# Optimization experiments

Measured on AMD Instinct MI355X. Metric: run time of the kernel, lower is better.

## Reference

```python
import jax, jax.numpy as jnp
import numpy as np

N = 100000      # nodes
E = 1600000     # edges (avg degree 16)
EMB = 64        # embedding_size (per-head out channels)
H = 2           # heads (hardcoded in module)
HID = 128       # hidden_size
NEG_SLOPE = 0.2 # GATv2 default


def setup_inputs() -> dict:
    key = jax.random.key(0)
    ks = jax.random.split(key, 12)
    s = 0.1
    x = jax.random.normal(ks[0], (N, 1), jnp.float32)
    edge_index = jax.random.randint(ks[1], (2, E), 0, N, dtype=jnp.int64)
    edge_attr = jax.random.normal(ks[2], (E, 1), jnp.float32)
    # GATv2Conv params (in_channels=1, out=EMB, heads=H, edge_dim=1)
    W_l = jax.random.normal(ks[3], (1, H * EMB), jnp.float32) * s
    b_l = jnp.zeros((H * EMB,), jnp.float32)
    W_r = jax.random.normal(ks[4], (1, H * EMB), jnp.float32) * s
    b_r = jnp.zeros((H * EMB,), jnp.float32)
    W_e = jax.random.normal(ks[5], (1, H * EMB), jnp.float32) * s   # lin_edge, bias=False
    att = jax.random.normal(ks[6], (H, EMB), jnp.float32) * s       # attention vector a
    bias_out = jnp.zeros((H * EMB,), jnp.float32)                   # conv output bias (concat=True)
    # fc: Linear(embedding_size*4, hidden_size)
    W_fc = jax.random.normal(ks[7], (HID, 4 * EMB), jnp.float32) * s
    b_fc = jnp.zeros((HID,), jnp.float32)
    return {
        "x": x, "edge_index": edge_index, "edge_attr": edge_attr,
        "target_node_idx": 123,
        "W_l": W_l, "b_l": b_l, "W_r": W_r, "b_r": b_r,
        "W_e": W_e, "att": att, "bias_out": bias_out,
        "W_fc": W_fc, "b_fc": b_fc,
    }


def reference(x, edge_index, edge_attr, target_node_idx,
              W_l, b_l, W_r, b_r, W_e, att, bias_out, W_fc, b_fc):
    n = x.shape[0]
    h, c = att.shape
    src, dst = edge_index[0], edge_index[1]

    # add_self_loops with fill_value='mean': per-target-node mean of incoming edge_attr
    deg = jax.ops.segment_sum(jnp.ones((src.shape[0],), x.dtype), dst, num_segments=n)
    attr_mean = jax.ops.segment_sum(edge_attr, dst, num_segments=n) / jnp.maximum(deg, 1.0)[:, None]
    loop = jnp.arange(n, dtype=src.dtype)
    src_f = jnp.concatenate([src, loop])
    dst_f = jnp.concatenate([dst, loop])
    ea = jnp.concatenate([edge_attr, attr_mean], axis=0)  # [E+N, 1]

    # per-head node transforms
    x_l = (x @ W_l + b_l).reshape(n, h, c)  # source transform
    x_r = (x @ W_r + b_r).reshape(n, h, c)  # target transform
    e_edge = (ea @ W_e).reshape(-1, h, c)   # edge-feature transform

    # GATv2: e_ij = a^T LeakyReLU(W_l x_j + W_r x_i + W_e e_ij)
    e = jax.nn.leaky_relu(x_l[src_f] + x_r[dst_f] + e_edge, NEG_SLOPE)  # [E', H, C]
    logits = jnp.einsum('ehc,hc->eh', e, att)  # [E', H]

    # segment softmax over incoming edges per target node
    m = jax.ops.segment_max(logits, dst_f, num_segments=n)     # [N, H]
    expv = jnp.exp(logits - m[dst_f])
    denom = jax.ops.segment_sum(expv, dst_f, num_segments=n)
    alpha = expv / denom[dst_f]                                 # [E', H]

    # weighted scatter-aggregate of source messages, concat heads, add bias
    out = jax.ops.segment_sum(alpha[:, :, None] * x_l[src_f], dst_f, num_segments=n)
    graph_emb = out.reshape(n, h * c) + bias_out                # [N, 2*EMB]

    # gather target, repeat, concat, linear
    tgt = graph_emb[target_node_idx]                            # [2*EMB]
    combined = jnp.concatenate([graph_emb, jnp.broadcast_to(tgt[None, :], graph_emb.shape)], axis=1)
    return combined @ W_fc.T + b_fc                             # [N, HID]
```

## Files before the change

### kernel.cpp

```cpp
#include <hip/hip_runtime.h>
#include <math.h>


#define LRELU_A1 0.6f
#define LRELU_A2 0.4f
#define NPB       512
#define NPB_SHIFT 9
#define EPB      2048
#define TB_BIN    512
#define CAP_MAX    24

__global__ void k_prep(const unsigned int* __restrict__ ei,
                       const float* __restrict__ att,
                       const float* __restrict__ W_l,
                       const float* __restrict__ b_l, const float* __restrict__ b_r,
                       const float* __restrict__ bias_out,
                       const float* __restrict__ W_fc, const float* __restrict__ b_fc,
                       float* __restrict__ C) {
  int j = threadIdx.x;
  unsigned long long nz = __ballot(j < 32 && ei[2 * j + 1] != 0u);
  if (j == 0) ((int*)C)[1024] = (nz == 0ull) ? 1 : 0;
  if (j >= 128) return;
  float a = att[j];
  C[j] = LRELU_A1 * a;
  C[128 + j] = LRELU_A2 * a;
  C[256 + j] = b_l[j] + b_r[j];
  const float* wrow = W_fc + j * 256;
  float u0 = 0.f, u1 = 0.f, v0 = 0.f, v1 = 0.f, cb = b_fc[j];
  for (int c = 0; c < 64; c++) {
    u0 = fmaf(W_l[c],      wrow[c],       u0);
    u1 = fmaf(W_l[64 + c], wrow[64 + c],  u1);
    v0 = fmaf(W_l[c],      wrow[128 + c], v0);
    v1 = fmaf(W_l[64 + c], wrow[192 + c], v1);
  }
  for (int t = 0; t < 128; t++) {
    float gb = b_l[t] + bias_out[t];
    cb = fmaf(gb, wrow[t] + wrow[128 + t], cb);
  }
  C[384 + j] = u0;
  C[512 + j] = u1;
  C[640 + j] = v0;
  C[768 + j] = v1;
  C[896 + j] = cb;
}

#define CH_STEP(comp, ACC, i)                                                      \
  do {                                                                             \
    float v_ = fmaf(xs4[i], wl.comp, fmaf(xt4[i], wr.comp, fmaf(ae4[i], we.comp, bb.comp))); \
    ACC[i] = fmaf(a2.comp, fabsf(v_), fmaf(a1.comp, v_, ACC[i]));                  \
  } while (0)

__global__ __launch_bounds__(TB_BIN) void k_bin(
    const float* __restrict__ x, const int* __restrict__ ei,
    const float* __restrict__ ea,
    const float* __restrict__ WL, const float* __restrict__ WR,
    const float* __restrict__ WE, const float* __restrict__ C,
    int4* __restrict__ rec, unsigned char* __restrict__ cntm,
    float* __restrict__ acc, int cap, int NB, int SB, int E) {
  __shared__ int cnt[256];
  const int tid = threadIdx.x;
  if (tid < 256) cnt[tid] = 0;
  __syncthreads();

  const int e0 = blockIdx.x * EPB;
  const bool w64 = ((const int*)C)[1024] != 0;
  const float* A1 = C;
  const float* A2 = C + 128;
  const float* BASE = C + 256;

  int de4[4];
  float ae4[4], xs4[4], xt4[4];
  bool ok[4];
#pragma unroll
  for (int i = 0; i < 4; i++) {
    int e = e0 + i * TB_BIN + tid;
    ok[i] = (e < E);
    int ee = ok[i] ? e : 0;
    int s_ = w64 ? ei[2 * ee] : ei[ee];
    int d_ = w64 ? ei[2 * (E + ee)] : ei[E + ee];
    de4[i] = d_;
    ae4[i] = ea[ee];
    xs4[i] = x[s_];
    xt4[i] = x[d_];
  }
  float acc0[4] = {0.f, 0.f, 0.f, 0.f};
  float acc1[4] = {0.f, 0.f, 0.f, 0.f};
#pragma unroll 4
  for (int jb = 0; jb < 64; jb += 4) {
    float4 wl = *(const float4*)(WL + jb);
    float4 wr = *(const float4*)(WR + jb);
    float4 we = *(const float4*)(WE + jb);
    float4 bb = *(const float4*)(BASE + jb);
    float4 a1 = *(const float4*)(A1 + jb);
    float4 a2 = *(const float4*)(A2 + jb);
#pragma unroll
    for (int i = 0; i < 4; i++) {
      CH_STEP(x, acc0, i); CH_STEP(y, acc0, i); CH_STEP(z, acc0, i); CH_STEP(w, acc0, i);
    }
  }
#pragma unroll 4
  for (int jb = 64; jb < 128; jb += 4) {
    float4 wl = *(const float4*)(WL + jb);
    float4 wr = *(const float4*)(WR + jb);
    float4 we = *(const float4*)(WE + jb);
    float4 bb = *(const float4*)(BASE + jb);
    float4 a1 = *(const float4*)(A1 + jb);
    float4 a2 = *(const float4*)(A2 + jb);
#pragma unroll
    for (int i = 0; i < 4; i++) {
      CH_STEP(x, acc1, i); CH_STEP(y, acc1, i); CH_STEP(z, acc1, i); CH_STEP(w, acc1, i);
    }
  }
#pragma unroll
  for (int i = 0; i < 4; i++) {
    if (!ok[i]) continue;
    int d_ = de4[i];
    int b = d_ >> NPB_SHIFT;
    float eh0 = __expf(acc0[i]);
    float eh1 = __expf(acc1[i]);
    int slot = atomicAdd(&cnt[b], 1);
    if (slot < cap) {
      unsigned eab = (__float_as_uint(ae4[i]) & ~511u) | (unsigned)(d_ & 511);
      rec[((size_t)b * SB + blockIdx.x) * cap + slot] =
          make_int4(__float_as_int(eh0), __float_as_int(eh1),
                    __float_as_int(xs4[i]), (int)eab);
    } else {
      float* a = acc + (size_t)d_ * 8;
      atomicAdd(a + 0, eh0);
      atomicAdd(a + 1, eh0 * xs4[i]);
      atomicAdd(a + 2, eh1);
      atomicAdd(a + 3, eh1 * xs4[i]);
      atomicAdd(a + 4, ae4[i]);
      atomicAdd(a + 5, 1.0f);
    }
  }
  __syncthreads();
  if (tid < 64) {
    unsigned w = 0;
#pragma unroll
    for (int k = 0; k < 4; k++) {
      int b = tid * 4 + k;
      unsigned c = (unsigned)min(cnt[b], cap);
      w |= (c & 0xFFu) << (8 * k);
    }
    ((unsigned*)(cntm + (size_t)blockIdx.x * 256))[tid] = w;
  }
}

__global__ __launch_bounds__(256, 4) void k_reduce(
    const int4* __restrict__ rec, const unsigned char* __restrict__ cntm,
    float* __restrict__ part, int cap, int SB) {
  __shared__ float lacc[NPB * 7];
  const int tid = threadIdx.x;
  const int b = blockIdx.x >> 1;
  const int j = blockIdx.x & 1;
  for (int i = tid; i < NPB * 7; i += 256) lacc[i] = 0.f;
  __syncthreads();
  const int sh = (SB + 1) >> 1;
  const int s_end = min(SB, (j + 1) * sh);
  for (int s = j * sh + tid; s < s_end; s += 256) {
    int c = cntm[(size_t)s * 256 + b];
    const int4* cell = rec + ((size_t)b * SB + s) * cap;
    for (int i = 0; i < c; i++) {
      int4 r = cell[i];
      float e0v = __int_as_float(r.x);
      float e1v = __int_as_float(r.y);
      float xsv = __int_as_float(r.z);
      unsigned eab = (unsigned)r.w;
      float* a = lacc + (int)(eab & 511u) * 7;
      float aev = __uint_as_float(eab & ~511u);
      atomicAdd(a + 0, e0v);
      atomicAdd(a + 1, e0v * xsv);
      atomicAdd(a + 2, e1v);
      atomicAdd(a + 3, e1v * xsv);
      atomicAdd(a + 4, aev);
      atomicAdd(a + 5, 1.0f);
    }
  }
  __syncthreads();
  float* dst = part + (size_t)blockIdx.x * (NPB * 6);
  for (int i = tid; i < NPB * 6; i += 256)
    dst[i] = lacc[(i / 6) * 7 + (i % 6)];
}

__global__ __launch_bounds__(256) void k_final(
    const float* __restrict__ x,
    const float* __restrict__ WL, const float* __restrict__ WR,
    const float* __restrict__ WE, const float* __restrict__ C,
    const float* __restrict__ part, const float* __restrict__ acc,
    float* __restrict__ S, int N) {
  int n = blockIdx.x * blockDim.x + threadIdx.x;
  if (n >= N) return;
  int b = n >> NPB_SHIFT;
  int l = n & (NPB - 1);
  const float* p0 = part + ((size_t)(2 * b)     * (NPB * 6)) + l * 6;
  const float* p1 = part + ((size_t)(2 * b + 1) * (NPB * 6)) + l * 6;
  const float* g  = acc + (size_t)n * 8;
  float den0 = p0[0] + p1[0] + g[0];
  float num0 = p0[1] + p1[1] + g[1];
  float den1 = p0[2] + p1[2] + g[2];
  float num1 = p0[3] + p1[3] + g[3];
  float asum = p0[4] + p1[4] + g[4];
  float cntv = p0[5] + p1[5] + g[5];
  const float* A1 = C;
  const float* A2 = C + 128;
  const float* BASE = C + 256;
  float xn = x[n];
  float am = asum / fmaxf(cntv, 1.0f);
  float acc0 = 0.f, acc1 = 0.f;
#pragma unroll 4
  for (int jb = 0; jb < 64; jb += 4) {
    float4 wl = *(const float4*)(WL + jb);
    float4 wr = *(const float4*)(WR + jb);
    float4 we = *(const float4*)(WE + jb);
    float4 bb = *(const float4*)(BASE + jb);
    float4 a1 = *(const float4*)(A1 + jb);
    float4 a2 = *(const float4*)(A2 + jb);
    float v;
    v = fmaf(xn, wl.x + wr.x, fmaf(am, we.x, bb.x)); acc0 = fmaf(a2.x, fabsf(v), fmaf(a1.x, v, acc0));
    v = fmaf(xn, wl.y + wr.y, fmaf(am, we.y, bb.y)); acc0 = fmaf(a2.y, fabsf(v), fmaf(a1.y, v, acc0));
    v = fmaf(xn, wl.z + wr.z, fmaf(am, we.z, bb.z)); acc0 = fmaf(a2.z, fabsf(v), fmaf(a1.z, v, acc0));
    v = fmaf(xn, wl.w + wr.w, fmaf(am, we.w, bb.w)); acc0 = fmaf(a2.w, fabsf(v), fmaf(a1.w, v, acc0));
  }
#pragma unroll 4
  for (int jb = 64; jb < 128; jb += 4) {
    float4 wl = *(const float4*)(WL + jb);
    float4 wr = *(const float4*)(WR + jb);
    float4 we = *(const float4*)(WE + jb);
    float4 bb = *(const float4*)(BASE + jb);
    float4 a1 = *(const float4*)(A1 + jb);
    float4 a2 = *(const float4*)(A2 + jb);
    float v;
    v = fmaf(xn, wl.x + wr.x, fmaf(am, we.x, bb.x)); acc1 = fmaf(a2.x, fabsf(v), fmaf(a1.x, v, acc1));
    v = fmaf(xn, wl.y + wr.y, fmaf(am, we.y, bb.y)); acc1 = fmaf(a2.y, fabsf(v), fmaf(a1.y, v, acc1));
    v = fmaf(xn, wl.z + wr.z, fmaf(am, we.z, bb.z)); acc1 = fmaf(a2.z, fabsf(v), fmaf(a1.z, v, acc1));
    v = fmaf(xn, wl.w + wr.w, fmaf(am, we.w, bb.w)); acc1 = fmaf(a2.w, fabsf(v), fmaf(a1.w, v, acc1));
  }
  float s0 = __expf(acc0), s1 = __expf(acc1);
  float2 sv;
  sv.x = (num0 + s0 * xn) / (den0 + s0);
  sv.y = (num1 + s1 * xn) / (den1 + s1);
  *(float2*)(S + 2 * n) = sv;
}

__global__ __launch_bounds__(256) void k_out(
    const float* __restrict__ S, const float* __restrict__ C,
    const int* __restrict__ tgtp, float* __restrict__ out, int N) {
  int g = blockIdx.x * blockDim.x + threadIdx.x;
  if (g >= N * 32) return;
  int n = g >> 5;
  int kq = (g & 31) * 4;
  int T = tgtp[0];
  float s0t = S[2 * T], s1t = S[2 * T + 1];
  float2 s = *(const float2*)(S + 2 * n);
  float4 u0 = *(const float4*)(C + 384 + kq);
  float4 u1 = *(const float4*)(C + 512 + kq);
  float4 v0 = *(const float4*)(C + 640 + kq);
  float4 v1 = *(const float4*)(C + 768 + kq);
  float4 cb = *(const float4*)(C + 896 + kq);
  float4 o;
  o.x = fmaf(s.x, u0.x, fmaf(s.y, u1.x, fmaf(s0t, v0.x, fmaf(s1t, v1.x, cb.x))));
  o.y = fmaf(s.x, u0.y, fmaf(s.y, u1.y, fmaf(s0t, v0.y, fmaf(s1t, v1.y, cb.y))));
  o.z = fmaf(s.x, u0.z, fmaf(s.y, u1.z, fmaf(s0t, v0.z, fmaf(s1t, v1.z, cb.z))));
  o.w = fmaf(s.x, u0.w, fmaf(s.y, u1.w, fmaf(s0t, v0.w, fmaf(s1t, v1.w, cb.w))));
  *(float4*)(out + n * 128 + kq) = o;
}

extern "C" void kernel_launch(void* const* d_in, const int* in_sizes, int n_in,
                              void* d_out, int out_size, void* d_ws, size_t ws_size,
                              hipStream_t stream) {
  const float* x        = (const float*)d_in[0];
  const int*   ei       = (const int*)d_in[1];
  const float* ea       = (const float*)d_in[2];
  const int*   tgt      = (const int*)d_in[3];
  const float* W_l      = (const float*)d_in[4];
  const float* b_l      = (const float*)d_in[5];
  const float* W_r      = (const float*)d_in[6];
  const float* b_r      = (const float*)d_in[7];
  const float* W_e      = (const float*)d_in[8];
  const float* att      = (const float*)d_in[9];
  const float* bias_out = (const float*)d_in[10];
  const float* W_fc     = (const float*)d_in[11];
  const float* b_fc     = (const float*)d_in[12];

  const int N = in_sizes[0];
  const int E = in_sizes[2];
  const int NB = (N + NPB - 1) / NPB;
  const int SB = (E + EPB - 1) / EPB;

  size_t cnt_bytes  = (size_t)SB * 256;
  size_t part_bytes = (size_t)NB * 2 * NPB * 6 * 4;
  size_t acc_bytes  = (size_t)N * 8 * 4;
  size_t S_bytes    = (size_t)N * 2 * 4;
  size_t C_bytes    = 1152 * 4;
  size_t fixed = cnt_bytes + part_bytes + acc_bytes + S_bytes + C_bytes + 1024;

  int cap = 1;
  if (ws_size > fixed) {
    size_t c = (ws_size - fixed) / ((size_t)NB * SB * 16);
    cap = (int)(c > CAP_MAX ? CAP_MAX : (c < 1 ? 1 : c));
  }

  char* p = (char*)d_ws;
  int4*          rec  = (int4*)p;          p += (size_t)NB * SB * cap * 16;
  unsigned char* cntm = (unsigned char*)p; p += cnt_bytes;
  float*         part = (float*)p;         p += part_bytes;
  float*         acc  = (float*)p;         p += acc_bytes;
  float*         S    = (float*)p;         p += S_bytes;
  float*         C    = (float*)p;

  hipMemsetAsync(acc, 0, acc_bytes, stream);
  k_prep<<<1, 128, 0, stream>>>((const unsigned int*)ei, att, W_l, b_l, b_r,
                                bias_out, W_fc, b_fc, C);
  k_bin<<<SB, TB_BIN, 0, stream>>>(x, ei, ea, W_l, W_r, W_e, C,
                                   rec, cntm, acc, cap, NB, SB, E);
  k_reduce<<<NB * 2, 256, 0, stream>>>(rec, cntm, part, cap, SB);
  k_final<<<(N + 255) / 256, 256, 0, stream>>>(x, W_l, W_r, W_e, C, part, acc, S, N);
  k_out<<<(N * 32 + 255) / 256, 256, 0, stream>>>(S, C, tgt, (float*)d_out, N);
}
```

Before: 240.7 us.

## Stage binned edge records in shared memory and flatten reduce over contiguous slots

k_bin now writes edge records into a shared-memory staging buffer per destination bin, then copies them out to global memory in one coalesced pass per bin, with a transposed count matrix. k_reduce is split four ways per bin and each thread walks a flat range of slots with four loads in flight, instead of one thread per source cell looping over a variable count. k_prep is parallelised across 1024 threads with shuffle reductions. The aim is to replace scattered record writes and divergent, latency-bound reduce loops with coalesced traffic, at the cost of a large shared buffer in k_bin that lowers its occupancy and one extra partial to sum in k_final.

After: 274.0 us. 1.14x slower.

```diff
diff --git a/kernel.cpp b/kernel.cpp
--- a/kernel.cpp
+++ b/kernel.cpp
@@ -8,40 +8,53 @@
 #define NPB_SHIFT 9
 #define EPB      2048
 #define TB_BIN    512
-#define CAP_MAX    24
-
-__global__ void k_prep(const unsigned int* __restrict__ ei,
-                       const float* __restrict__ att,
-                       const float* __restrict__ W_l,
-                       const float* __restrict__ b_l, const float* __restrict__ b_r,
-                       const float* __restrict__ bias_out,
-                       const float* __restrict__ W_fc, const float* __restrict__ b_fc,
-                       float* __restrict__ C) {
-  int j = threadIdx.x;
-  unsigned long long nz = __ballot(j < 32 && ei[2 * j + 1] != 0u);
-  if (j == 0) ((int*)C)[1024] = (nz == 0ull) ? 1 : 0;
-  if (j >= 128) return;
-  float a = att[j];
-  C[j] = LRELU_A1 * a;
-  C[128 + j] = LRELU_A2 * a;
-  C[256 + j] = b_l[j] + b_r[j];
+#define CAPL       24
+#define NBMAX     200
+#define SPLITS      4
+
+__global__ __launch_bounds__(1024) void k_prep(
+    const unsigned int* __restrict__ ei,
+    const float* __restrict__ att, const float* __restrict__ W_l,
+    const float* __restrict__ b_l, const float* __restrict__ b_r,
+    const float* __restrict__ bias_out,
+    const float* __restrict__ W_fc, const float* __restrict__ b_fc,
+    float* __restrict__ C) {
+  int t = threadIdx.x;
+  unsigned long long nz = __ballot(t < 32 && ei[2 * t + 1] != 0u);
+  if (t == 0) ((int*)C)[1024] = (nz == 0ull) ? 1 : 0;
+  int j = t >> 3, q = t & 7;
   const float* wrow = W_fc + j * 256;
-  float u0 = 0.f, u1 = 0.f, v0 = 0.f, v1 = 0.f, cb = b_fc[j];
-  for (int c = 0; c < 64; c++) {
-    u0 = fmaf(W_l[c],      wrow[c],       u0);
-    u1 = fmaf(W_l[64 + c], wrow[64 + c],  u1);
-    v0 = fmaf(W_l[c],      wrow[128 + c], v0);
-    v1 = fmaf(W_l[64 + c], wrow[192 + c], v1);
-  }
-  for (int t = 0; t < 128; t++) {
-    float gb = b_l[t] + bias_out[t];
-    cb = fmaf(gb, wrow[t] + wrow[128 + t], cb);
-  }
-  C[384 + j] = u0;
-  C[512 + j] = u1;
-  C[640 + j] = v0;
-  C[768 + j] = v1;
-  C[896 + j] = cb;
+  float u0 = 0.f, u1 = 0.f, v0 = 0.f, v1 = 0.f, cb = 0.f;
+  for (int c = q; c < 64; c += 8) {
+    float wl0 = W_l[c], wl1 = W_l[64 + c];
+    u0 = fmaf(wl0, wrow[c],       u0);
+    u1 = fmaf(wl1, wrow[64 + c],  u1);
+    v0 = fmaf(wl0, wrow[128 + c], v0);
+    v1 = fmaf(wl1, wrow[192 + c], v1);
+  }
+  for (int c = q; c < 128; c += 8) {
+    float gb = b_l[c] + bias_out[c];
+    cb = fmaf(gb, wrow[c] + wrow[128 + c], cb);
+  }
+#pragma unroll
+  for (int off = 4; off; off >>= 1) {
+    u0 += __shfl_down(u0, off);
+    u1 += __shfl_down(u1, off);
+    v0 += __shfl_down(v0, off);
+    v1 += __shfl_down(v1, off);
+    cb += __shfl_down(cb, off);
+  }
+  if (q == 0) {
+    float a = att[j];
+    C[j]       = LRELU_A1 * a;
+    C[128 + j] = LRELU_A2 * a;
+    C[256 + j] = b_l[j] + b_r[j];
+    C[384 + j] = u0;
+    C[512 + j] = u1;
+    C[640 + j] = v0;
+    C[768 + j] = v1;
+    C[896 + j] = cb + b_fc[j];
+  }
 }
 
 #define CH_STEP(comp, ACC, i)                                                      \
@@ -56,10 +69,11 @@
     const float* __restrict__ WL, const float* __restrict__ WR,
     const float* __restrict__ WE, const float* __restrict__ C,
     int4* __restrict__ rec, unsigned char* __restrict__ cntm,
-    float* __restrict__ acc, int cap, int NB, int SB, int E) {
-  __shared__ int cnt[256];
+    float* __restrict__ acc, int capG, int NB, int SB, int E) {
+  __shared__ int4 stag[NBMAX * CAPL];
+  __shared__ int  cnt[NBMAX];
   const int tid = threadIdx.x;
-  if (tid < 256) cnt[tid] = 0;
+  for (int i = tid; i < NBMAX; i += TB_BIN) cnt[i] = 0;
   __syncthreads();
 
   const int e0 = blockIdx.x * EPB;
@@ -118,12 +132,11 @@
     int b = d_ >> NPB_SHIFT;
     float eh0 = __expf(acc0[i]);
     float eh1 = __expf(acc1[i]);
-    int slot = atomicAdd(&cnt[b], 1);
-    if (slot < cap) {
+    int slot = (b < NBMAX) ? atomicAdd(&cnt[b], 1) : CAPL;
+    if (slot < CAPL) {
       unsigned eab = (__float_as_uint(ae4[i]) & ~511u) | (unsigned)(d_ & 511);
-      rec[((size_t)b * SB + blockIdx.x) * cap + slot] =
-          make_int4(__float_as_int(eh0), __float_as_int(eh1),
-                    __float_as_int(xs4[i]), (int)eab);
+      stag[b * CAPL + slot] = make_int4(__float_as_int(eh0), __float_as_int(eh1),
+                                        __float_as_int(xs4[i]), (int)eab);
     } else {
       float* a = acc + (size_t)d_ * 8;
       atomicAdd(a + 0, eh0);
@@ -135,47 +148,81 @@
     }
   }
   __syncthreads();
-  if (tid < 64) {
-    unsigned w = 0;
-#pragma unroll
-    for (int k = 0; k < 4; k++) {
-      int b = tid * 4 + k;
-      unsigned c = (unsigned)min(cnt[b], cap);
-      w |= (c & 0xFFu) << (8 * k);
-    }
-    ((unsigned*)(cntm + (size_t)blockIdx.x * 256))[tid] = w;
-  }
-}
-
-__global__ __launch_bounds__(256, 4) void k_reduce(
-    const int4* __restrict__ rec, const unsigned char* __restrict__ cntm,
-    float* __restrict__ part, int cap, int SB) {
-  __shared__ float lacc[NPB * 7];
-  const int tid = threadIdx.x;
-  const int b = blockIdx.x >> 1;
-  const int j = blockIdx.x & 1;
-  for (int i = tid; i < NPB * 7; i += 256) lacc[i] = 0.f;
-  __syncthreads();
-  const int sh = (SB + 1) >> 1;
-  const int s_end = min(SB, (j + 1) * sh);
-  for (int s = j * sh + tid; s < s_end; s += 256) {
-    int c = cntm[(size_t)s * 256 + b];
-    const int4* cell = rec + ((size_t)b * SB + s) * cap;
-    for (int i = 0; i < c; i++) {
-      int4 r = cell[i];
-      float e0v = __int_as_float(r.x);
-      float e1v = __int_as_float(r.y);
+  for (int b = tid; b < NB; b += TB_BIN)
+    cntm[(size_t)b * SB + blockIdx.x] = (unsigned char)min(cnt[b], capG);
+  const int tot = NB * CAPL;
+  for (int g = tid; g < tot; g += TB_BIN) {
+    int b = (g * 10923) >> 18;
+    int slot = g - b * 24;
+    int c = cnt[b];
+    int cG = min(c, capG);
+    if (slot < cG) {
+      rec[((size_t)b * SB + blockIdx.x) * capG + slot] = stag[g];
+    } else if (slot < min(c, CAPL)) {
+      int4 r = stag[g];
+      int dst = (b << NPB_SHIFT) | (r.w & 511);
+      float eh0 = __int_as_float(r.x);
+      float eh1 = __int_as_float(r.y);
       float xsv = __int_as_float(r.z);
-      unsigned eab = (unsigned)r.w;
-      float* a = lacc + (int)(eab & 511u) * 7;
-      float aev = __uint_as_float(eab & ~511u);
-      atomicAdd(a + 0, e0v);
-      atomicAdd(a + 1, e0v * xsv);
-      atomicAdd(a + 2, e1v);
-      atomicAdd(a + 3, e1v * xsv);
+      float aev = __uint_as_float(((unsigned)r.w) & ~511u);
+      float* a = acc + (size_t)dst * 8;
+      atomicAdd(a + 0, eh0);
+      atomicAdd(a + 1, eh0 * xsv);
+      atomicAdd(a + 2, eh1);
+      atomicAdd(a + 3, eh1 * xsv);
       atomicAdd(a + 4, aev);
       atomicAdd(a + 5, 1.0f);
     }
+  }
+}
+
+__device__ __forceinline__ void red_step(float* lacc, const unsigned char* cl,
+                                         int4 r, int i, int M, int capG) {
+  int s_rel = (i * M) >> 18;
+  int slot = i - s_rel * capG;
+  if (slot < (int)cl[s_rel]) {
+    float e0v = __int_as_float(r.x);
+    float e1v = __int_as_float(r.y);
+    float xsv = __int_as_float(r.z);
+    unsigned eab = (unsigned)r.w;
+    float* a = lacc + (int)(eab & 511u) * 7;
+    atomicAdd(a + 0, e0v);
+    atomicAdd(a + 1, e0v * xsv);
+    atomicAdd(a + 2, e1v);
+    atomicAdd(a + 3, e1v * xsv);
+    atomicAdd(a + 4, __uint_as_float(eab & ~511u));
+    atomicAdd(a + 5, 1.0f);
+  }
+}
+
+__global__ __launch_bounds__(256) void k_reduce(
+    const int4* __restrict__ rec, const unsigned char* __restrict__ cntm,
+    float* __restrict__ part, int capG, int M, int SB) {
+  __shared__ float lacc[NPB * 7];
+  __shared__ unsigned char cl[256];
+  const int tid = threadIdx.x;
+  const int b = blockIdx.x >> 2;
+  const int q = blockIdx.x & 3;
+  const int sh = (SB + SPLITS - 1) / SPLITS;
+  const int s0 = q * sh;
+  const int nseg = min(sh, SB - s0);
+  for (int i = tid; i < NPB * 7; i += 256) lacc[i] = 0.f;
+  for (int i = tid; i < nseg; i += 256) cl[i] = cntm[(size_t)b * SB + s0 + i];
+  __syncthreads();
+  const int4* row = rec + ((size_t)b * SB + s0) * capG;
+  const int nslots = nseg * capG;
+  for (int base = tid; base < nslots; base += 1024) {
+    int i1 = base + 256, i2 = base + 512, i3 = base + 768;
+    bool v1 = i1 < nslots, v2 = i2 < nslots, v3 = i3 < nslots;
+    int4 r0 = row[base];
+    int4 r1, r2, r3;
+    if (v1) r1 = row[i1];
+    if (v2) r2 = row[i2];
+    if (v3) r3 = row[i3];
+    red_step(lacc, cl, r0, base, M, capG);
+    if (v1) red_step(lacc, cl, r1, i1, M, capG);
+    if (v2) red_step(lacc, cl, r2, i2, M, capG);
+    if (v3) red_step(lacc, cl, r3, i3, M, capG);
   }
   __syncthreads();
   float* dst = part + (size_t)blockIdx.x * (NPB * 6);
@@ -193,15 +240,15 @@
   if (n >= N) return;
   int b = n >> NPB_SHIFT;
   int l = n & (NPB - 1);
-  const float* p0 = part + ((size_t)(2 * b)     * (NPB * 6)) + l * 6;
-  const float* p1 = part + ((size_t)(2 * b + 1) * (NPB * 6)) + l * 6;
-  const float* g  = acc + (size_t)n * 8;
-  float den0 = p0[0] + p1[0] + g[0];
-  float num0 = p0[1] + p1[1] + g[1];
-  float den1 = p0[2] + p1[2] + g[2];
-  float num1 = p0[3] + p1[3] + g[3];
-  float asum = p0[4] + p1[4] + g[4];
-  float cntv = p0[5] + p1[5] + g[5];
+  const float* p = part + (size_t)(b * 4) * (NPB * 6) + l * 6;
+  const float* g = acc + (size_t)n * 8;
+  float v0 = p[0] + p[3072] + p[6144] + p[9216] + g[0];
+  float v1 = p[1] + p[3073] + p[6145] + p[9217] + g[1];
+  float v2 = p[2] + p[3074] + p[6146] + p[9218] + g[2];
+  float v3 = p[3] + p[3075] + p[6147] + p[9219] + g[3];
+  float v4 = p[4] + p[3076] + p[6148] + p[9220] + g[4];
+  float v5 = p[5] + p[3077] + p[6149] + p[9221] + g[5];
+  float den0 = v0, num0 = v1, den1 = v2, num1 = v3, asum = v4, cntv = v5;
   const float* A1 = C;
   const float* A2 = C + 128;
   const float* BASE = C + 256;
@@ -285,24 +332,25 @@
 
   const int N = in_sizes[0];
   const int E = in_sizes[2];
-  const int NB = (N + NPB - 1) / NPB;
+  const int NB = (N + NPB - 1) >> NPB_SHIFT;
   const int SB = (E + EPB - 1) / EPB;
 
-  size_t cnt_bytes  = (size_t)SB * 256;
-  size_t part_bytes = (size_t)NB * 2 * NPB * 6 * 4;
+  size_t cnt_bytes  = (((size_t)NB * SB) + 15) & ~(size_t)15;
+  size_t part_bytes = (size_t)NB * SPLITS * NPB * 6 * 4;
   size_t acc_bytes  = (size_t)N * 8 * 4;
-  size_t S_bytes    = (size_t)N * 2 * 4;
+  size_t S_bytes    = (((size_t)N * 2 * 4) + 15) & ~(size_t)15;
   size_t C_bytes    = 1152 * 4;
-  size_t fixed = cnt_bytes + part_bytes + acc_bytes + S_bytes + C_bytes + 1024;
-
-  int cap = 1;
+  size_t fixed = cnt_bytes + part_bytes + acc_bytes + S_bytes + C_bytes + 64;
+
+  int capG = 1;
   if (ws_size > fixed) {
     size_t c = (ws_size - fixed) / ((size_t)NB * SB * 16);
-    cap = (int)(c > CAP_MAX ? CAP_MAX : (c < 1 ? 1 : c));
-  }
+    capG = (int)(c > CAPL ? CAPL : (c < 1 ? 1 : c));
+  }
+  int M = (int)((262144 + capG - 1) / capG);
 
   char* p = (char*)d_ws;
-  int4*          rec  = (int4*)p;          p += (size_t)NB * SB * cap * 16;
+  int4*          rec  = (int4*)p;          p += (size_t)NB * SB * capG * 16;
   unsigned char* cntm = (unsigned char*)p; p += cnt_bytes;
   float*         part = (float*)p;         p += part_bytes;
   float*         acc  = (float*)p;         p += acc_bytes;
@@ -310,11 +358,11 @@
   float*         C    = (float*)p;
 
   hipMemsetAsync(acc, 0, acc_bytes, stream);
-  k_prep<<<1, 128, 0, stream>>>((const unsigned int*)ei, att, W_l, b_l, b_r,
-                                bias_out, W_fc, b_fc, C);
+  k_prep<<<1, 1024, 0, stream>>>((const unsigned int*)ei, att, W_l, b_l, b_r,
+                                 bias_out, W_fc, b_fc, C);
   k_bin<<<SB, TB_BIN, 0, stream>>>(x, ei, ea, W_l, W_r, W_e, C,
-                                   rec, cntm, acc, cap, NB, SB, E);
-  k_reduce<<<NB * 2, 256, 0, stream>>>(rec, cntm, part, cap, SB);
+                                   rec, cntm, acc, capG, NB, SB, E);
+  k_reduce<<<NB * SPLITS, 256, 0, stream>>>(rec, cntm, part, capG, M, SB);
   k_final<<<(N + 255) / 256, 256, 0, stream>>>(x, W_l, W_r, W_e, C, part, acc, S, N);
   k_out<<<(N * 32 + 255) / 256, 256, 0, stream>>>(S, C, tgt, (float*)d_out, N);
 }
```
